# Kernel tuning notes

Hardware: AMD Instinct MI355X
Metric: run time of the kernel (lower is better)

Reference implementation:

```python
import jax, jax.numpy as jnp
import numpy as np

VIS_DIM = 4096
HIDDEN_D = 4096
EMB_DIM = 512
B = 128
N_NEG = 2048


def setup_inputs() -> dict:
    key = jax.random.key(0)
    k = jax.random.split(key, 7)
    vfs = jax.random.normal(k[0], (B, VIS_DIM), dtype=jnp.float32)
    p_lfs = jax.random.normal(k[1], (B, EMB_DIM), dtype=jnp.float32)
    n_lfs = jax.random.normal(k[2], (N_NEG, EMB_DIM), dtype=jnp.float32)
    # Linear params (PyTorch layout: W [out, in], y = x @ W.T + b)
    s_h = 1.0 / np.sqrt(VIS_DIM)
    s_e = 1.0 / np.sqrt(HIDDEN_D)
    W_h = jax.random.uniform(k[3], (HIDDEN_D, VIS_DIM), jnp.float32, -s_h, s_h)
    b_h = jax.random.uniform(k[4], (HIDDEN_D,), jnp.float32, -s_h, s_h)
    W_e = jax.random.uniform(k[5], (EMB_DIM, HIDDEN_D), jnp.float32, -s_e, s_e)
    b_e = jax.random.uniform(k[6], (EMB_DIM,), jnp.float32, -s_e, s_e)
    return {"vfs": vfs, "p_lfs": p_lfs, "n_lfs": n_lfs,
            "W_h": W_h, "b_h": b_h, "W_e": W_e, "b_e": b_e}


def _partial_order_sim(hypers, hypos):
    # -||relu(hypers - hypos)||_2 reduced over the last axis
    act = jax.nn.relu(hypers - hypos)
    return -jnp.sqrt(jnp.sum(act * act, axis=-1))


def reference(vfs, p_lfs, n_lfs, W_h, b_h, W_e, b_e):
    # Two plain Linears (NO ReLU in between, matching the original forward)
    vf_hidden = vfs @ W_h.T + b_h            # [B, 4096]
    vf_emb = vf_hidden @ W_e.T + b_e          # [B, emb]
    # positive score per sample
    p_scores = _partial_order_sim(p_lfs, vf_emb)                    # [B]
    # negative scores, batched over all samples at once (replaces per-sample loop)
    n_scores = _partial_order_sim(n_lfs[None, :, :], vf_emb[:, None, :])  # [B, N]
    score_stack = jnp.concatenate([p_scores[:, None], n_scores], axis=1)  # [B, N+1]
    return score_stack
```

## Files before the change

### kernel.cpp

```cpp
#include <hip/hip_runtime.h>
#include <hip/hip_bf16.h>

#define B_N  128
#define VIS  4096
#define HID  4096
#define EMB  512
#define NNEG 2048
#define OUTN (NNEG + 1)
#define SPLIT1 8

using f32x4  = __attribute__((ext_vector_type(4))) float;
using bf16x8 = __attribute__((ext_vector_type(8))) short;

static __device__ __forceinline__ unsigned pk2bf(float x, float y) {
  union { __hip_bfloat162 h; unsigned u; } c;
  c.h = __float22bfloat162_rn(make_float2(x, y));
  return c.u;
}

#define PIPE_BARRIER() __asm__ volatile("s_waitcnt lgkmcnt(0)\n\ts_barrier" ::: "memory")

__global__ __launch_bounds__(256) void prep_kernel(
    const float* __restrict__ src, unsigned short* __restrict__ dst,
    float* __restrict__ emb) {
  const int idx = blockIdx.x * 256 + threadIdx.x;
  float4 a = ((const float4*)src)[idx * 2];
  float4 b = ((const float4*)src)[idx * 2 + 1];
  uint4 pk;
  pk.x = pk2bf(a.x, a.y); pk.y = pk2bf(a.z, a.w);
  pk.z = pk2bf(b.x, b.y); pk.w = pk2bf(b.z, b.w);
  ((uint4*)dst)[idx] = pk;
  if (idx < (B_N * EMB / 4))
    ((float4*)emb)[idx] = make_float4(0.f, 0.f, 0.f, 0.f);
}

__global__ __launch_bounds__(512, 4) void gemm1_kernel(
    const unsigned short* __restrict__ Abf, const float* __restrict__ Wh,
    const float* __restrict__ bh, float* __restrict__ Hp) {
  const int n0    = blockIdx.x * 32;
  const int kbase = blockIdx.y * 512;

  __shared__ __align__(16) unsigned short Ws[2][32 * 64];

  const int t = threadIdx.x, w = t >> 6, lane = t & 63;
  const int m_lane = lane & 15, kq = lane >> 4;
  f32x4 acc[2] = {};

  const int wr = t >> 4, Gw = (t & 15) >> 1, sub = (t & 1) * 4;
  const float* Wg = Wh + (size_t)(n0 + wr) * VIS + kbase + (t & 15) * 4;
  const int wofs = wr * 64 + ((Gw ^ (wr & 7)) * 8) + sub;

  const unsigned short* Ag = Abf + (size_t)(w * 16 + m_lane) * VIS + kbase + kq * 8;

  float4 wv[3];
  bf16x8 av[3][2];

  wv[0] = *(const float4*)(Wg);
  wv[1] = *(const float4*)(Wg + 64);
  wv[2] = *(const float4*)(Wg + 128);
  av[0][0] = *(const bf16x8*)(Ag);
  av[0][1] = *(const bf16x8*)(Ag + 32);
  av[1][0] = *(const bf16x8*)(Ag + 64);
  av[1][1] = *(const bf16x8*)(Ag + 96);
  {
    uint2 pk = make_uint2(pk2bf(wv[0].x, wv[0].y), pk2bf(wv[0].z, wv[0].w));
    *(uint2*)&Ws[0][wofs] = pk;
  }
  PIPE_BARRIER();

#pragma unroll
  for (int k = 0; k < 8; ++k) {
    const int cur = k & 1;
    if (k + 3 < 8) wv[k % 3] = *(const float4*)(Wg + (k + 3) * 64);
    if (k + 2 < 8) {
      av[(k + 2) % 3][0] = *(const bf16x8*)(Ag + (k + 2) * 64);
      av[(k + 2) % 3][1] = *(const bf16x8*)(Ag + (k + 2) * 64 + 32);
    }
    if (k + 1 < 8) {
      const float4 wc = wv[(k + 1) % 3];
      uint2 pk = make_uint2(pk2bf(wc.x, wc.y), pk2bf(wc.z, wc.w));
      *(uint2*)&Ws[1 - cur][wofs] = pk;
    }
#pragma unroll
    for (int ks = 0; ks < 2; ++ks) {
      const int Gk = ks * 4 + kq;
      const int cA = m_lane, cB = m_lane + 16;
      bf16x8 b0 = *(const bf16x8*)&Ws[cur][cA * 64 + ((Gk ^ (cA & 7)) * 8)];
      bf16x8 b1 = *(const bf16x8*)&Ws[cur][cB * 64 + ((Gk ^ (cB & 7)) * 8)];
      acc[0] = __builtin_amdgcn_mfma_f32_16x16x32_bf16(av[k % 3][ks], b0, acc[0], 0, 0, 0);
      acc[1] = __builtin_amdgcn_mfma_f32_16x16x32_bf16(av[k % 3][ks], b1, acc[1], 0, 0, 0);
    }
    PIPE_BARRIER();
  }

  float* Pd = Hp + (size_t)blockIdx.y * (B_N * HID);
  const int rq = (lane >> 4) * 4;
#pragma unroll
  for (int ni = 0; ni < 2; ++ni) {
    const int ng = n0 + ni * 16 + m_lane;
    const float bias = (blockIdx.y == 0) ? bh[ng] : 0.0f;
#pragma unroll
    for (int r = 0; r < 4; ++r)
      Pd[(size_t)(w * 16 + rq + r) * HID + ng] = acc[ni][r] + bias;
  }
}

__global__ __launch_bounds__(256) void cvt_kernel(
    const float* __restrict__ Hp, unsigned short* __restrict__ dst) {
  const int idx = blockIdx.x * 256 + threadIdx.x;
  const size_t PS = (size_t)B_N * HID;
  float4 a = ((const float4*)Hp)[idx * 2];
  float4 b = ((const float4*)Hp)[idx * 2 + 1];
#pragma unroll
  for (int p = 1; p < SPLIT1; ++p) {
    float4 ap = ((const float4*)(Hp + p * PS))[idx * 2];
    float4 bp = ((const float4*)(Hp + p * PS))[idx * 2 + 1];
    a.x += ap.x; a.y += ap.y; a.z += ap.z; a.w += ap.w;
    b.x += bp.x; b.y += bp.y; b.z += bp.z; b.w += bp.w;
  }
  uint4 pk;
  pk.x = pk2bf(a.x, a.y); pk.y = pk2bf(a.z, a.w);
  pk.z = pk2bf(b.x, b.y); pk.w = pk2bf(b.z, b.w);
  ((uint4*)dst)[idx] = pk;
}

__global__ __launch_bounds__(512, 4) void gemm2_kernel(
    const unsigned short* __restrict__ Hbf, const float* __restrict__ We,
    const float* __restrict__ be, float* __restrict__ emb) {
  const int n0    = blockIdx.x * 16;
  const int kbase = blockIdx.y * 512;

  __shared__ __align__(16) unsigned short Ws[2][16 * 64];

  const int t = threadIdx.x, w = t >> 6, lane = t & 63;
  const int m_lane = lane & 15, kq = lane >> 4;
  f32x4 acc = {};

  const int wr = t >> 5, e = (t & 31) * 2;
  const float* Wg = We + (size_t)(n0 + wr) * HID + kbase + e;
  const int wofs = wr * 64 + (((e >> 3) ^ (wr & 7)) * 8) + (e & 7);

  const unsigned short* Ag = Hbf + (size_t)(w * 16 + m_lane) * HID + kbase + kq * 8;

  float2 wv[3];
  bf16x8 av[3][2];

  wv[0] = *(const float2*)(Wg);
  wv[1] = *(const float2*)(Wg + 64);
  wv[2] = *(const float2*)(Wg + 128);
  av[0][0] = *(const bf16x8*)(Ag);
  av[0][1] = *(const bf16x8*)(Ag + 32);
  av[1][0] = *(const bf16x8*)(Ag + 64);
  av[1][1] = *(const bf16x8*)(Ag + 96);
  *(unsigned*)&Ws[0][wofs] = pk2bf(wv[0].x, wv[0].y);
  PIPE_BARRIER();

#pragma unroll
  for (int k = 0; k < 8; ++k) {
    const int cur = k & 1;
    if (k + 3 < 8) wv[k % 3] = *(const float2*)(Wg + (k + 3) * 64);
    if (k + 2 < 8) {
      av[(k + 2) % 3][0] = *(const bf16x8*)(Ag + (k + 2) * 64);
      av[(k + 2) % 3][1] = *(const bf16x8*)(Ag + (k + 2) * 64 + 32);
    }
    if (k + 1 < 8) {
      const float2 wc = wv[(k + 1) % 3];
      *(unsigned*)&Ws[1 - cur][wofs] = pk2bf(wc.x, wc.y);
    }
#pragma unroll
    for (int ks = 0; ks < 2; ++ks) {
      const int Gk = ks * 4 + kq;
      bf16x8 b0 = *(const bf16x8*)&Ws[cur][m_lane * 64 + ((Gk ^ (m_lane & 7)) * 8)];
      acc = __builtin_amdgcn_mfma_f32_16x16x32_bf16(av[k % 3][ks], b0, acc, 0, 0, 0);
    }
    PIPE_BARRIER();
  }

  const int rq = (lane >> 4) * 4;
  const int ng = n0 + m_lane;
  const float bias = (blockIdx.y == 0) ? be[ng] : 0.0f;
#pragma unroll
  for (int r = 0; r < 4; ++r)
    atomicAdd(&emb[(w * 16 + rq + r) * EMB + ng], acc[r] + bias);
}

__global__ __launch_bounds__(256, 2) void score_kernel(
    const float* __restrict__ emb, const float* __restrict__ n_lfs,
    const float* __restrict__ p_lfs, float* __restrict__ out) {
  const int bx = blockIdx.x;
  const int t = threadIdx.x;
  const int s = t & 15, tb = t >> 4;

  if (bx < 1024) {
    const int nc = bx >> 3, bt = bx & 7;
    const int n0 = nc * 16, b0 = bt * 16;
    __shared__ __align__(16) float nl[16 * 576];
#pragma unroll
    for (int i = 0; i < 8; ++i) {
      const int f = t + i * 256;
      const int r = f >> 7, o4 = f & 127;
      float4 v = *(const float4*)(n_lfs + (size_t)(n0 + r) * EMB + o4 * 4);
      *(float4*)&nl[r * 576 + (o4 >> 3) * 36 + (o4 & 7) * 4] = v;
    }
    const float* eb = emb + (size_t)(b0 + tb) * EMB + s * 32;
    float4 ev[8];
#pragma unroll
    for (int i = 0; i < 8; ++i) ev[i] = *(const float4*)(eb + i * 4);
    __syncthreads();

    for (int j = 0; j < 16; ++j) {
      const float* nr = &nl[j * 576 + s * 36];
      float a0 = 0.f, a1 = 0.f, a2 = 0.f, a3 = 0.f;
#pragma unroll
      for (int i = 0; i < 8; ++i) {
        float4 nv = *(const float4*)(nr + i * 4);
        float d0 = fmaxf(nv.x - ev[i].x, 0.f);
        float d1 = fmaxf(nv.y - ev[i].y, 0.f);
        float d2 = fmaxf(nv.z - ev[i].z, 0.f);
        float d3 = fmaxf(nv.w - ev[i].w, 0.f);
        a0 = fmaf(d0, d0, a0); a1 = fmaf(d1, d1, a1);
        a2 = fmaf(d2, d2, a2); a3 = fmaf(d3, d3, a3);
      }
      float ss = (a0 + a1) + (a2 + a3);
      ss += __shfl_xor(ss, 1);
      ss += __shfl_xor(ss, 2);
      ss += __shfl_xor(ss, 4);
      ss += __shfl_xor(ss, 8);
      if (s == 0) out[(size_t)(b0 + tb) * OUTN + 1 + n0 + j] = -sqrtf(ss);
    }
  } else {
    const int b = (bx - 1024) * 16 + tb;
    const float* eb = emb + (size_t)b * EMB + s * 32;
    const float* pb = p_lfs + (size_t)b * EMB + s * 32;
    float a0 = 0.f, a1 = 0.f, a2 = 0.f, a3 = 0.f;
#pragma unroll
    for (int i = 0; i < 8; ++i) {
      float4 pv = *(const float4*)(pb + i * 4);
      float4 ev = *(const float4*)(eb + i * 4);
      float d0 = fmaxf(pv.x - ev.x, 0.f);
      float d1 = fmaxf(pv.y - ev.y, 0.f);
      float d2 = fmaxf(pv.z - ev.z, 0.f);
      float d3 = fmaxf(pv.w - ev.w, 0.f);
      a0 = fmaf(d0, d0, a0); a1 = fmaf(d1, d1, a1);
      a2 = fmaf(d2, d2, a2); a3 = fmaf(d3, d3, a3);
    }
    float ss = (a0 + a1) + (a2 + a3);
    ss += __shfl_xor(ss, 1);
    ss += __shfl_xor(ss, 2);
    ss += __shfl_xor(ss, 4);
    ss += __shfl_xor(ss, 8);
    if (s == 0) out[(size_t)b * OUTN] = -sqrtf(ss);
  }
}

extern "C" void kernel_launch(void* const* d_in, const int* in_sizes, int n_in,
                              void* d_out, int out_size, void* d_ws, size_t ws_size,
                              hipStream_t stream) {
  const float* vfs   = (const float*)d_in[0];
  const float* p_lfs = (const float*)d_in[1];
  const float* n_lfs = (const float*)d_in[2];
  const float* W_h   = (const float*)d_in[3];
  const float* b_h   = (const float*)d_in[4];
  const float* W_e   = (const float*)d_in[5];
  const float* b_e   = (const float*)d_in[6];
  float* out = (float*)d_out;

  char* ws = (char*)d_ws;
  float*          Hp  = (float*)ws;
  float*          emb = (float*)(ws + (16u << 20));
  unsigned short* Abf = (unsigned short*)(ws + (16u << 20) + (256u << 10));
  unsigned short* Hbf = (unsigned short*)(ws + (17u << 20) + (256u << 10));

  prep_kernel<<<256, 256, 0, stream>>>(vfs, Abf, emb);
  gemm1_kernel<<<dim3(HID / 32, SPLIT1), 512, 0, stream>>>(Abf, W_h, b_h, Hp);
  cvt_kernel<<<256, 256, 0, stream>>>(Hp, Hbf);
  gemm2_kernel<<<dim3(EMB / 16, 8), 512, 0, stream>>>(Hbf, W_e, b_e, emb);
  score_kernel<<<1032, 256, 0, stream>>>(emb, n_lfs, p_lfs, out);
}
```

Baseline: 162.7 us.

## Widen gemm1 N-tile to 64 and prefetch all weight loads up front

gemm1 now has each block cover 64 output columns instead of 32. This halves the grid to 512 blocks and reuses each A fragment across four MFMAs. Both gemm1 and gemm2 now issue every fp32 weight load for the block's K-slice at kernel start instead of a 3-deep rolling prefetch, putting more memory requests in flight for the bandwidth-bound W_h stream. The cost is many more live registers (16 float4 per thread in gemm1) and fewer blocks, which may reduce occupancy under the 512x4 launch bound.

```diff
diff --git a/kernel.cpp b/kernel.cpp
--- a/kernel.cpp
+++ b/kernel.cpp
@@ -37,58 +37,65 @@
 __global__ __launch_bounds__(512, 4) void gemm1_kernel(
     const unsigned short* __restrict__ Abf, const float* __restrict__ Wh,
     const float* __restrict__ bh, float* __restrict__ Hp) {
-  const int n0    = blockIdx.x * 32;
+  const int n0    = blockIdx.x * 64;
   const int kbase = blockIdx.y * 512;
 
-  __shared__ __align__(16) unsigned short Ws[2][32 * 64];
+  __shared__ __align__(16) unsigned short Ws[2][64 * 64];
 
   const int t = threadIdx.x, w = t >> 6, lane = t & 63;
   const int m_lane = lane & 15, kq = lane >> 4;
-  f32x4 acc[2] = {};
-
-  const int wr = t >> 4, Gw = (t & 15) >> 1, sub = (t & 1) * 4;
-  const float* Wg = Wh + (size_t)(n0 + wr) * VIS + kbase + (t & 15) * 4;
-  const int wofs = wr * 64 + ((Gw ^ (wr & 7)) * 8) + sub;
+  f32x4 acc[4] = {};
+
+  const int wr = t >> 3, wg = t & 7;
+  const float* Wg = Wh + (size_t)(n0 + wr) * VIS + kbase + wg * 8;
+  const int wofs = wr * 64 + ((wg ^ (wr & 7)) * 8);
 
   const unsigned short* Ag = Abf + (size_t)(w * 16 + m_lane) * VIS + kbase + kq * 8;
 
-  float4 wv[3];
+  float4 wva[8], wvb[8];
+#pragma unroll
+  for (int i = 0; i < 8; ++i) {
+    wva[i] = *(const float4*)(Wg + i * 64);
+    wvb[i] = *(const float4*)(Wg + i * 64 + 4);
+  }
+
   bf16x8 av[3][2];
-
-  wv[0] = *(const float4*)(Wg);
-  wv[1] = *(const float4*)(Wg + 64);
-  wv[2] = *(const float4*)(Wg + 128);
   av[0][0] = *(const bf16x8*)(Ag);
   av[0][1] = *(const bf16x8*)(Ag + 32);
   av[1][0] = *(const bf16x8*)(Ag + 64);
   av[1][1] = *(const bf16x8*)(Ag + 96);
+
   {
-    uint2 pk = make_uint2(pk2bf(wv[0].x, wv[0].y), pk2bf(wv[0].z, wv[0].w));
-    *(uint2*)&Ws[0][wofs] = pk;
+    uint4 pk;
+    pk.x = pk2bf(wva[0].x, wva[0].y); pk.y = pk2bf(wva[0].z, wva[0].w);
+    pk.z = pk2bf(wvb[0].x, wvb[0].y); pk.w = pk2bf(wvb[0].z, wvb[0].w);
+    *(uint4*)&Ws[0][wofs] = pk;
   }
   PIPE_BARRIER();
 
 #pragma unroll
   for (int k = 0; k < 8; ++k) {
     const int cur = k & 1;
-    if (k + 3 < 8) wv[k % 3] = *(const float4*)(Wg + (k + 3) * 64);
     if (k + 2 < 8) {
       av[(k + 2) % 3][0] = *(const bf16x8*)(Ag + (k + 2) * 64);
       av[(k + 2) % 3][1] = *(const bf16x8*)(Ag + (k + 2) * 64 + 32);
     }
     if (k + 1 < 8) {
-      const float4 wc = wv[(k + 1) % 3];
-      uint2 pk = make_uint2(pk2bf(wc.x, wc.y), pk2bf(wc.z, wc.w));
-      *(uint2*)&Ws[1 - cur][wofs] = pk;
+      uint4 pk;
+      pk.x = pk2bf(wva[k + 1].x, wva[k + 1].y); pk.y = pk2bf(wva[k + 1].z, wva[k + 1].w);
+      pk.z = pk2bf(wvb[k + 1].x, wvb[k + 1].y); pk.w = pk2bf(wvb[k + 1].z, wvb[k + 1].w);
+      *(uint4*)&Ws[1 - cur][wofs] = pk;
     }
 #pragma unroll
     for (int ks = 0; ks < 2; ++ks) {
       const int Gk = ks * 4 + kq;
-      const int cA = m_lane, cB = m_lane + 16;
-      bf16x8 b0 = *(const bf16x8*)&Ws[cur][cA * 64 + ((Gk ^ (cA & 7)) * 8)];
-      bf16x8 b1 = *(const bf16x8*)&Ws[cur][cB * 64 + ((Gk ^ (cB & 7)) * 8)];
-      acc[0] = __builtin_amdgcn_mfma_f32_16x16x32_bf16(av[k % 3][ks], b0, acc[0], 0, 0, 0);
-      acc[1] = __builtin_amdgcn_mfma_f32_16x16x32_bf16(av[k % 3][ks], b1, acc[1], 0, 0, 0);
+      const bf16x8 a = av[k % 3][ks];
+#pragma unroll
+      for (int ni = 0; ni < 4; ++ni) {
+        const int c = m_lane + ni * 16;
+        bf16x8 b = *(const bf16x8*)&Ws[cur][c * 64 + ((Gk ^ (c & 7)) * 8)];
+        acc[ni] = __builtin_amdgcn_mfma_f32_16x16x32_bf16(a, b, acc[ni], 0, 0, 0);
+      }
     }
     PIPE_BARRIER();
   }
@@ -96,7 +103,7 @@
   float* Pd = Hp + (size_t)blockIdx.y * (B_N * HID);
   const int rq = (lane >> 4) * 4;
 #pragma unroll
-  for (int ni = 0; ni < 2; ++ni) {
+  for (int ni = 0; ni < 4; ++ni) {
     const int ng = n0 + ni * 16 + m_lane;
     const float bias = (blockIdx.y == 0) ? bh[ng] : 0.0f;
 #pragma unroll
@@ -142,29 +149,28 @@
 
   const unsigned short* Ag = Hbf + (size_t)(w * 16 + m_lane) * HID + kbase + kq * 8;
 
-  float2 wv[3];
+  float2 wv[8];
+#pragma unroll
+  for (int i = 0; i < 8; ++i) wv[i] = *(const float2*)(Wg + i * 64);
+
   bf16x8 av[3][2];
-
-  wv[0] = *(const float2*)(Wg);
-  wv[1] = *(const float2*)(Wg + 64);
-  wv[2] = *(const float2*)(Wg + 128);
   av[0][0] = *(const bf16x8*)(Ag);
   av[0][1] = *(const bf16x8*)(Ag + 32);
   av[1][0] = *(const bf16x8*)(Ag + 64);
   av[1][1] = *(const bf16x8*)(Ag + 96);
+
   *(unsigned*)&Ws[0][wofs] = pk2bf(wv[0].x, wv[0].y);
   PIPE_BARRIER();
 
 #pragma unroll
   for (int k = 0; k < 8; ++k) {
     const int cur = k & 1;
-    if (k + 3 < 8) wv[k % 3] = *(const float2*)(Wg + (k + 3) * 64);
     if (k + 2 < 8) {
       av[(k + 2) % 3][0] = *(const bf16x8*)(Ag + (k + 2) * 64);
       av[(k + 2) % 3][1] = *(const bf16x8*)(Ag + (k + 2) * 64 + 32);
     }
     if (k + 1 < 8) {
-      const float2 wc = wv[(k + 1) % 3];
+      const float2 wc = wv[k + 1];
       *(unsigned*)&Ws[1 - cur][wofs] = pk2bf(wc.x, wc.y);
     }
 #pragma unroll
@@ -272,7 +278,7 @@
   unsigned short* Hbf = (unsigned short*)(ws + (17u << 20) + (256u << 10));
 
   prep_kernel<<<256, 256, 0, stream>>>(vfs, Abf, emb);
-  gemm1_kernel<<<dim3(HID / 32, SPLIT1), 512, 0, stream>>>(Abf, W_h, b_h, Hp);
+  gemm1_kernel<<<dim3(HID / 64, SPLIT1), 512, 0, stream>>>(Abf, W_h, b_h, Hp);
   cvt_kernel<<<256, 256, 0, stream>>>(Hp, Hbf);
   gemm2_kernel<<<dim3(EMB / 16, 8), 512, 0, stream>>>(Hbf, W_e, b_e, emb);
   score_kernel<<<1032, 256, 0, stream>>>(emb, n_lfs, p_lfs, out);
```

After: 155.6 us. -4.3%, faster.
